# Optimization experiments

Measured on AMD Instinct MI355X. Metric: run time of the kernel, lower is better.

## Reference

```python
import jax, jax.numpy as jnp
import numpy as np

ROTARY_DIM = 32
THETA = 10000.0

def _rotate_half(t):
    # interleaved pairs: (..., d) -> rotate each (x1, x2) pair to (-x2, x1)
    x = t.reshape(t.shape[:-1] + (-1, 2))
    x1, x2 = x[..., 0], x[..., 1]
    return jnp.stack([-x2, x1], axis=-1).reshape(t.shape)

def _apply_rope(t, offset=0):
    # t: (B, h, T, dh); rotate only the first ROTARY_DIM dims
    T = t.shape[-2]
    inv_freq = 1.0 / (THETA ** (jnp.arange(0, ROTARY_DIM, 2, dtype=jnp.float32) / ROTARY_DIM))
    pos = jnp.arange(T, dtype=jnp.float32) + offset
    freqs = pos[:, None] * inv_freq[None, :]                 # (T, ROTARY_DIM/2)
    freqs = jnp.repeat(freqs, 2, axis=-1)                    # (T, ROTARY_DIM) interleaved
    cos, sin = jnp.cos(freqs), jnp.sin(freqs)
    t_rot, t_pass = t[..., :ROTARY_DIM], t[..., ROTARY_DIM:]
    t_rot = t_rot * cos + _rotate_half(t_rot) * sin
    return jnp.concatenate([t_rot, t_pass], axis=-1)

def setup_inputs() -> dict:
    key = jax.random.key(0)
    k1, k2, k3 = jax.random.split(key, 3)
    B, T, dim = 4, 1024, 1024
    x = jax.random.normal(k1, (B, T, dim), dtype=jnp.float32)
    Wqkv = jax.random.normal(k2, (dim, 3 * dim), dtype=jnp.float32) * (dim ** -0.5)
    Wout = jax.random.normal(k3, (dim, dim), dtype=jnp.float32) * (dim ** -0.5)
    return {"x": x, "Wqkv": Wqkv, "Wout": Wout}

def reference(x, Wqkv, Wout):
    B, T, dim = x.shape
    n_heads = 16
    dh = dim // n_heads
    qkv = x @ Wqkv                                            # (B, T, 3*dim)
    qkv = qkv.reshape(B, T, 3, n_heads, dh)
    qkv = jnp.transpose(qkv, (2, 0, 3, 1, 4))                 # (3, B, h, T, dh)
    q, k, v = qkv[0], qkv[1], qkv[2]
    q = _apply_rope(q, offset=0)
    k = _apply_rope(k, offset=0)
    scale = 1.0 / jnp.sqrt(jnp.asarray(dh, dtype=x.dtype))
    scores = jnp.einsum('bhqd,bhkd->bhqk', q, k) * scale      # (B, h, T, T)
    causal = jnp.tril(jnp.ones((T, T), dtype=bool))
    scores = jnp.where(causal, scores, jnp.asarray(-jnp.inf, dtype=scores.dtype))
    attn = jax.nn.softmax(scores, axis=-1)
    out = jnp.einsum('bhqk,bhkd->bhqd', attn, v)              # (B, h, T, dh)
    out = jnp.transpose(out, (0, 2, 1, 3)).reshape(B, T, dim)
    return out @ Wout
```

## Files before the change

kernel.cpp:

```cpp
#include <hip/hip_runtime.h>
#include <cstdint>
#include <cstddef>

typedef __bf16 bf16;
typedef __bf16 bf16x4 __attribute__((ext_vector_type(4)));
typedef __bf16 bf16x8 __attribute__((ext_vector_type(8)));
typedef float f32x4 __attribute__((ext_vector_type(4)));

#define DEVINL __device__ __forceinline__

static constexpr int Tn   = 1024;
static constexpr int DIM  = 1024;
static constexpr int NH   = 16;
static constexpr int DH   = 64;
static constexpr int QKVN = 3072;

DEVINL void g2l16(const void* g, void* l) {
  __builtin_amdgcn_global_load_lds(
      (const __attribute__((address_space(1))) void*)g,
      (__attribute__((address_space(3))) void*)l, 16, 0, 0);
}

__global__ void k_prep(const float* __restrict__ x, bf16* __restrict__ xb,
                       float2* __restrict__ tab,
                       const float* __restrict__ w1, bf16* __restrict__ o1,
                       const float* __restrict__ w2, bf16* __restrict__ o2) {
  __shared__ float tile[32][33];
  int bx = blockIdx.x;
  if (bx < 4096) {
    int i = bx * 256 + threadIdx.x;
    float4 v = reinterpret_cast<const float4*>(x)[i];
    bf16 o[4] = {(bf16)v.x, (bf16)v.y, (bf16)v.z, (bf16)v.w};
    reinterpret_cast<uint2*>(xb)[i] = *reinterpret_cast<uint2*>(o);
    return;
  }
  if (bx < 4160) {
    int e = (bx - 4096) * 256 + threadIdx.x;
    int t = e >> 4, fi = e & 15;
    float inv = exp2f(-(float)fi * 0.830482023721841f);
    float sn, cs;
    sincosf((float)t * inv, &sn, &cs);
    tab[e] = make_float2(cs, sn);
    return;
  }
  int sub = bx - 4160;
  const float* in; bf16* out; int N, n0, k0;
  if (sub < 3072) { in = w1; out = o1; N = 3072; n0 = (sub % 96) * 32; k0 = (sub / 96) * 32; }
  else { sub -= 3072; in = w2; out = o2; N = 1024; n0 = (sub & 31) * 32; k0 = (sub >> 5) * 32; }
  int tx = threadIdx.x & 31, ty = threadIdx.x >> 5;
#pragma unroll
  for (int j = 0; j < 32; j += 8)
    tile[ty + j][tx] = in[(size_t)(k0 + ty + j) * N + n0 + tx];
  __syncthreads();
#pragma unroll
  for (int j = 0; j < 32; j += 8)
    out[(size_t)(n0 + ty + j) * 1024 + k0 + tx] = (bf16)tile[tx][ty + j];
}

template <bool F32OUT, int BN, bool ROPE>
__global__ __launch_bounds__(256) void k_gemm_bt(
    const bf16* __restrict__ A, const bf16* __restrict__ Bt,
    void* __restrict__ Cp, bf16* __restrict__ vt, const float2* __restrict__ tab,
    int M, int N, int K) {
  constexpr int NI = BN / 32;
  constexpr int NB = BN / 32;
  __shared__ bf16 As[128 * 64];
  __shared__ bf16 Bs[BN * 64];
  const int tid  = threadIdx.x;
  const int wave = tid >> 6, lane = tid & 63;
  const int lrow = lane & 15, quad = lane >> 4;
  const int m0 = blockIdx.y * 128, n0 = blockIdx.x * BN;
  const int wm = (wave >> 1) * 64, wn = (wave & 1) * (BN / 2);

  const bf16* aP[4];
  const bf16* bP[NB];
#pragma unroll
  for (int i = 0; i < 4; i++) {
    int li = i * 256 + tid;
    int row = li >> 3, c = li & 7, gc = c ^ (row & 7);
    aP[i] = A + (size_t)(m0 + row) * K + gc * 8;
  }
#pragma unroll
  for (int i = 0; i < NB; i++) {
    int li = i * 256 + tid;
    int row = li >> 3, c = li & 7, gc = c ^ (row & 7);
    bP[i] = Bt + (size_t)(n0 + row) * K + gc * 8;
  }

  f32x4 acc[4][NI];
#pragma unroll
  for (int mi = 0; mi < 4; mi++)
#pragma unroll
    for (int ni = 0; ni < NI; ni++) acc[mi][ni] = 0.f;

  for (int k0 = 0; k0 < K; k0 += 64) {
    __syncthreads();
#pragma unroll
    for (int i = 0; i < 4; i++) {
      g2l16(aP[i], As + (i * 256 + tid) * 8);
      aP[i] += 64;
    }
#pragma unroll
    for (int i = 0; i < NB; i++) {
      g2l16(bP[i], Bs + (i * 256 + tid) * 8);
      bP[i] += 64;
    }
    __syncthreads();
#pragma unroll
    for (int ki = 0; ki < 2; ki++) {
      bf16x8 af[4], bfr[NI];
#pragma unroll
      for (int mi = 0; mi < 4; mi++) {
        int r = wm + mi * 16 + lrow;
        int pc = (ki * 4 + quad) ^ (r & 7);
        af[mi] = *reinterpret_cast<const bf16x8*>(As + r * 64 + pc * 8);
      }
#pragma unroll
      for (int ni = 0; ni < NI; ni++) {
        int r = wn + ni * 16 + lrow;
        int pc = (ki * 4 + quad) ^ (r & 7);
        bfr[ni] = *reinterpret_cast<const bf16x8*>(Bs + r * 64 + pc * 8);
      }
#pragma unroll
      for (int mi = 0; mi < 4; mi++)
#pragma unroll
        for (int ni = 0; ni < NI; ni++)
          acc[mi][ni] = __builtin_amdgcn_mfma_f32_16x16x32_bf16(bfr[ni], af[mi], acc[mi][ni], 0, 0, 0);
    }
  }

#pragma unroll
  for (int mi = 0; mi < 4; mi++) {
    const int row = m0 + wm + mi * 16 + lrow;
#pragma unroll
    for (int ni = 0; ni < NI; ni++) {
      const int colb = n0 + wn + ni * 16 + quad * 4;
      f32x4 v = acc[mi][ni];
      if (ROPE && colb >= 2 * DIM) {
        int t = row & (Tn - 1), bb = row >> 10;
        int hdb = colb - 2 * DIM;
#pragma unroll
        for (int r = 0; r < 4; r++)
          vt[((size_t)((bb << 10) + hdb + r) << 10) + t] = (bf16)v[r];
        continue;
      }
      if (ROPE && ((colb & 63) < 32)) {
        int t = row & (Tn - 1);
        int fi0 = (colb >> 1) & 15;
        float2 c0 = tab[(t << 4) + fi0];
        float2 c1 = tab[(t << 4) + fi0 + 1];
        float a0 = v[0], a1 = v[1], a2 = v[2], a3 = v[3];
        v[0] = a0 * c0.x - a1 * c0.y;
        v[1] = a1 * c0.x + a0 * c0.y;
        v[2] = a2 * c1.x - a3 * c1.y;
        v[3] = a3 * c1.x + a2 * c1.y;
      }
      if (F32OUT) {
        float4 st = {v[0], v[1], v[2], v[3]};
        *reinterpret_cast<float4*>(reinterpret_cast<float*>(Cp) + (size_t)row * N + colb) = st;
      } else {
        bf16x4 pk;
#pragma unroll
        for (int r = 0; r < 4; r++) pk[r] = (bf16)v[r];
        *reinterpret_cast<bf16x4*>(reinterpret_cast<bf16*>(Cp) + (size_t)row * N + colb) = pk;
      }
    }
  }
}

__global__ __launch_bounds__(256) void k_attn(
    const bf16* __restrict__ qkv, const bf16* __restrict__ vt,
    bf16* __restrict__ ao) {
  __shared__ bf16 Ks[2][64 * 64];
  __shared__ bf16 Vs[2][64 * 64];
  __shared__ bf16 Ps[4][16 * 64];

  const int tid  = threadIdx.x;
  const int wave = tid >> 6, lane = tid & 63;
  const int lrow = lane & 15, quad = lane >> 4;
  const int bh = blockIdx.y, b = bh >> 4, h = bh & 15;
  const int jn = blockIdx.x;
  const int jf = 15 - jn;
  const int qwf = jf * 64 + wave * 16;
  const int qwn = jn * 64 + wave * 16;
  const size_t qbase = (size_t)b * Tn * QKVN;

  bf16x8 qff[2], qfn[2];
  {
    const float SC = 0.125f * 1.44269504088896f;
    const bf16* qpf = qkv + qbase + (size_t)(qwf + lrow) * QKVN + h * DH;
    const bf16* qpn = qkv + qbase + (size_t)(qwn + lrow) * QKVN + h * DH;
    qff[0] = *reinterpret_cast<const bf16x8*>(qpf + quad * 8);
    qff[1] = *reinterpret_cast<const bf16x8*>(qpf + 32 + quad * 8);
    qfn[0] = *reinterpret_cast<const bf16x8*>(qpn + quad * 8);
    qfn[1] = *reinterpret_cast<const bf16x8*>(qpn + 32 + quad * 8);
#pragma unroll
    for (int j = 0; j < 8; j++) {
      qff[0][j] = (bf16)((float)qff[0][j] * SC);
      qff[1][j] = (bf16)((float)qff[1][j] * SC);
      qfn[0][j] = (bf16)((float)qfn[0][j] * SC);
      qfn[1][j] = (bf16)((float)qfn[1][j] * SC);
    }
  }

  f32x4 oaf[4], oan[4];
#pragma unroll
  for (int g = 0; g < 4; g++) { oaf[g] = 0.f; oan[g] = 0.f; }
  float lif = 0.f, lin = 0.f;

  const int ntiles = jf + 1;

  auto stage = [&](int k0, int bufi) {
#pragma unroll
    for (int i = 0; i < 2; i++) {
      int li2 = i * 256 + tid;
      int row = li2 >> 3, c = li2 & 7;
      int gc = c ^ (row & 7);
      g2l16(qkv + qbase + (size_t)(k0 + row) * QKVN + DIM + h * DH + gc * 8,
            &Ks[bufi][li2 * 8]);
      g2l16(vt + ((size_t)bh * DH + row) * Tn + k0 + gc * 8,
            &Vs[bufi][li2 * 8]);
    }
  };

  auto unit = [&](const bf16* ks, const bf16* vs, bf16x8 (&qf)[2], f32x4 (&oa)[4],
                  float& li, bool diag) {
    f32x4 s[4];
#pragma unroll
    for (int g = 0; g < 4; g++) s[g] = 0.f;
#pragma unroll
    for (int kh = 0; kh < 2; kh++) {
      const int cX = ((kh * 4 + quad) ^ (lrow & 7)) << 3;
#pragma unroll
      for (int g = 0; g < 4; g++) {
        bf16x8 kf = *reinterpret_cast<const bf16x8*>(ks + (g * 16 + lrow) * 64 + cX);
        s[g] = __builtin_amdgcn_mfma_f32_16x16x32_bf16(kf, qf[kh], s[g], 0, 0, 0);
      }
    }
    float psum = 0.f;
    const int qrel = wave * 16 + lrow;
#pragma unroll
    for (int g = 0; g < 4; g++) {
      bf16x4 pk;
#pragma unroll
      for (int r = 0; r < 4; r++) {
        float p = exp2f(s[g][r]);
        if (diag) {
          int kl = g * 16 + quad * 4 + r;
          p = (kl <= qrel) ? p : 0.f;
        }
        psum += p;
        pk[r] = (bf16)p;
      }
      int chunk = 2 * g + (quad >> 1);
      *reinterpret_cast<bf16x4*>(
          Ps[wave] + lrow * 64 + ((chunk ^ (lrow & 7)) << 3) + 4 * (quad & 1)) = pk;
    }
    li += psum;
#pragma unroll
    for (int kh = 0; kh < 2; kh++) {
      const int cX = ((kh * 4 + quad) ^ (lrow & 7)) << 3;
      bf16x8 pf = *reinterpret_cast<const bf16x8*>(Ps[wave] + lrow * 64 + cX);
#pragma unroll
      for (int g = 0; g < 4; g++) {
        bf16x8 vf = *reinterpret_cast<const bf16x8*>(vs + (g * 16 + lrow) * 64 + cX);
        oa[g] = __builtin_amdgcn_mfma_f32_16x16x32_bf16(pf, vf, oa[g], 0, 0, 0);
      }
    }
  };

  stage(0, 0);

  for (int kt = 0; kt < ntiles; kt++) {
    const int buf = kt & 1;
    __syncthreads();
    if (kt + 1 < ntiles) stage((kt + 1) << 6, buf ^ 1);

    const bf16* ks = Ks[buf];
    const bf16* vs = Vs[buf];

    unit(ks, vs, qff, oaf, lif, kt == jf);
    if (kt <= jn)
      unit(ks, vs, qfn, oan, lin, kt == jn);
  }

  lif += __shfl_xor(lif, 16, 64); lif += __shfl_xor(lif, 32, 64);
  lin += __shfl_xor(lin, 16, 64); lin += __shfl_xor(lin, 32, 64);

#pragma unroll
  for (int r = 0; r < 4; r++) {
    int m = quad * 4 + r;
    float invf = 1.0f / __shfl(lif, m, 64);
    float invn = 1.0f / __shfl(lin, m, 64);
    bf16* dstf = ao + ((size_t)b * Tn + qwf + m) * DIM + h * DH;
    bf16* dstn = ao + ((size_t)b * Tn + qwn + m) * DIM + h * DH;
    dstf[ 0 + lrow] = (bf16)(oaf[0][r] * invf);
    dstf[16 + lrow] = (bf16)(oaf[1][r] * invf);
    dstf[32 + lrow] = (bf16)(oaf[2][r] * invf);
    dstf[48 + lrow] = (bf16)(oaf[3][r] * invf);
    dstn[ 0 + lrow] = (bf16)(oan[0][r] * invn);
    dstn[16 + lrow] = (bf16)(oan[1][r] * invn);
    dstn[32 + lrow] = (bf16)(oan[2][r] * invn);
    dstn[48 + lrow] = (bf16)(oan[3][r] * invn);
  }
}

extern "C" void kernel_launch(void* const* d_in, const int* in_sizes, int n_in,
                              void* d_out, int out_size, void* d_ws, size_t ws_size,
                              hipStream_t stream) {
  const float* x    = (const float*)d_in[0];
  const float* Wqkv = (const float*)d_in[1];
  const float* Wout = (const float*)d_in[2];
  char* ws = (char*)d_ws;

  bf16*   xb    = (bf16*)(ws + 0);
  bf16*   wqkvT = (bf16*)(ws + 8388608);
  bf16*   woutT = (bf16*)(ws + 14680064);
  bf16*   qkv   = (bf16*)(ws + 16777216);
  bf16*   vt    = (bf16*)(ws + 41943040);
  bf16*   ao    = (bf16*)(ws + 50331648);
  float2* tab   = (float2*)(ws + 58720256);

  k_prep<<<8256, 256, 0, stream>>>(x, xb, tab, Wqkv, wqkvT, Wout, woutT);
  k_gemm_bt<false, 96, true><<<dim3(32, 32), 256, 0, stream>>>(
      xb, wqkvT, (void*)qkv, vt, tab, 4096, 3072, 1024);
  k_attn<<<dim3(8, 64), 256, 0, stream>>>(qkv, vt, ao);
  k_gemm_bt<true, 64, false><<<dim3(16, 32), 256, 0, stream>>>(
      ao, woutT, d_out, nullptr, nullptr, 4096, 1024, 1024);
  (void)in_sizes; (void)n_in; (void)out_size; (void)ws_size;
}
```

Measured before the change: 169.2 us.

## Split attention blocks into far/near wave pairs with 32-row query tiles

The attention kernel now handles two 32-row query tiles per block (one far, one near, each served by two waves) instead of two 64-row tiles processed by every wave. The grid doubles to 16x64 blocks, and each wave does only one unit per K/V tile, skipping compute once its own causal range is done. This gives more blocks and shorter per-block work, at the cost of loading K/V tiles twice as often per query row and leaving near waves idle during later iterations. Separately, the QKV GEMM tile width changes from 96 to 128 with a matching grid change.

```diff
diff --git a/kernel.cpp b/kernel.cpp
--- a/kernel.cpp
+++ b/kernel.cpp
@@ -180,35 +180,34 @@
   const int lrow = lane & 15, quad = lane >> 4;
   const int bh = blockIdx.y, b = bh >> 4, h = bh & 15;
   const int jn = blockIdx.x;
-  const int jf = 15 - jn;
-  const int qwf = jf * 64 + wave * 16;
-  const int qwn = jn * 64 + wave * 16;
+  const int jf = 31 - jn;
+  const bool isFar = wave < 2;
+  const int jmine = isFar ? jf : jn;
+  const int swave = wave & 1;
+  const int qw = jmine * 32 + swave * 16;
   const size_t qbase = (size_t)b * Tn * QKVN;
 
-  bf16x8 qff[2], qfn[2];
+  const int ntf = (jf >> 1) + 1;
+  const int myNt = (isFar ? ntf : ((jn >> 1) + 1));
+  const int qrel = (jmine & 1) * 32 + swave * 16 + lrow;
+
+  bf16x8 qf[2];
   {
     const float SC = 0.125f * 1.44269504088896f;
-    const bf16* qpf = qkv + qbase + (size_t)(qwf + lrow) * QKVN + h * DH;
-    const bf16* qpn = qkv + qbase + (size_t)(qwn + lrow) * QKVN + h * DH;
-    qff[0] = *reinterpret_cast<const bf16x8*>(qpf + quad * 8);
-    qff[1] = *reinterpret_cast<const bf16x8*>(qpf + 32 + quad * 8);
-    qfn[0] = *reinterpret_cast<const bf16x8*>(qpn + quad * 8);
-    qfn[1] = *reinterpret_cast<const bf16x8*>(qpn + 32 + quad * 8);
+    const bf16* qp = qkv + qbase + (size_t)(qw + lrow) * QKVN + h * DH;
+    qf[0] = *reinterpret_cast<const bf16x8*>(qp + quad * 8);
+    qf[1] = *reinterpret_cast<const bf16x8*>(qp + 32 + quad * 8);
 #pragma unroll
     for (int j = 0; j < 8; j++) {
-      qff[0][j] = (bf16)((float)qff[0][j] * SC);
-      qff[1][j] = (bf16)((float)qff[1][j] * SC);
-      qfn[0][j] = (bf16)((float)qfn[0][j] * SC);
-      qfn[1][j] = (bf16)((float)qfn[1][j] * SC);
-    }
-  }
-
-  f32x4 oaf[4], oan[4];
-#pragma unroll
-  for (int g = 0; g < 4; g++) { oaf[g] = 0.f; oan[g] = 0.f; }
-  float lif = 0.f, lin = 0.f;
-
-  const int ntiles = jf + 1;
+      qf[0][j] = (bf16)((float)qf[0][j] * SC);
+      qf[1][j] = (bf16)((float)qf[1][j] * SC);
+    }
+  }
+
+  f32x4 oa[4];
+#pragma unroll
+  for (int g = 0; g < 4; g++) oa[g] = 0.f;
+  float li = 0.f;
 
   auto stage = [&](int k0, int bufi) {
 #pragma unroll
@@ -223,85 +222,77 @@
     }
   };
 
-  auto unit = [&](const bf16* ks, const bf16* vs, bf16x8 (&qf)[2], f32x4 (&oa)[4],
-                  float& li, bool diag) {
-    f32x4 s[4];
-#pragma unroll
-    for (int g = 0; g < 4; g++) s[g] = 0.f;
-#pragma unroll
-    for (int kh = 0; kh < 2; kh++) {
-      const int cX = ((kh * 4 + quad) ^ (lrow & 7)) << 3;
-#pragma unroll
-      for (int g = 0; g < 4; g++) {
-        bf16x8 kf = *reinterpret_cast<const bf16x8*>(ks + (g * 16 + lrow) * 64 + cX);
-        s[g] = __builtin_amdgcn_mfma_f32_16x16x32_bf16(kf, qf[kh], s[g], 0, 0, 0);
-      }
-    }
-    float psum = 0.f;
-    const int qrel = wave * 16 + lrow;
-#pragma unroll
-    for (int g = 0; g < 4; g++) {
-      bf16x4 pk;
-#pragma unroll
-      for (int r = 0; r < 4; r++) {
-        float p = exp2f(s[g][r]);
-        if (diag) {
-          int kl = g * 16 + quad * 4 + r;
-          p = (kl <= qrel) ? p : 0.f;
-        }
-        psum += p;
-        pk[r] = (bf16)p;
-      }
-      int chunk = 2 * g + (quad >> 1);
-      *reinterpret_cast<bf16x4*>(
-          Ps[wave] + lrow * 64 + ((chunk ^ (lrow & 7)) << 3) + 4 * (quad & 1)) = pk;
-    }
-    li += psum;
-#pragma unroll
-    for (int kh = 0; kh < 2; kh++) {
-      const int cX = ((kh * 4 + quad) ^ (lrow & 7)) << 3;
-      bf16x8 pf = *reinterpret_cast<const bf16x8*>(Ps[wave] + lrow * 64 + cX);
-#pragma unroll
-      for (int g = 0; g < 4; g++) {
-        bf16x8 vf = *reinterpret_cast<const bf16x8*>(vs + (g * 16 + lrow) * 64 + cX);
-        oa[g] = __builtin_amdgcn_mfma_f32_16x16x32_bf16(pf, vf, oa[g], 0, 0, 0);
-      }
-    }
-  };
-
   stage(0, 0);
 
-  for (int kt = 0; kt < ntiles; kt++) {
+  for (int kt = 0; kt < ntf; kt++) {
     const int buf = kt & 1;
     __syncthreads();
-    if (kt + 1 < ntiles) stage((kt + 1) << 6, buf ^ 1);
-
-    const bf16* ks = Ks[buf];
-    const bf16* vs = Vs[buf];
-
-    unit(ks, vs, qff, oaf, lif, kt == jf);
-    if (kt <= jn)
-      unit(ks, vs, qfn, oan, lin, kt == jn);
-  }
-
-  lif += __shfl_xor(lif, 16, 64); lif += __shfl_xor(lif, 32, 64);
-  lin += __shfl_xor(lin, 16, 64); lin += __shfl_xor(lin, 32, 64);
+    if (kt + 1 < ntf) stage((kt + 1) << 6, buf ^ 1);
+
+    if (kt < myNt) {
+      const bf16* ks = Ks[buf];
+      const bf16* vs = Vs[buf];
+      const bool diag = (kt == myNt - 1);
+
+      f32x4 s[4];
+#pragma unroll
+      for (int g = 0; g < 4; g++) s[g] = 0.f;
+#pragma unroll
+      for (int kh = 0; kh < 2; kh++) {
+        const int cX = ((kh * 4 + quad) ^ (lrow & 7)) << 3;
+#pragma unroll
+        for (int g = 0; g < 4; g++) {
+          bf16x8 kf = *reinterpret_cast<const bf16x8*>(ks + (g * 16 + lrow) * 64 + cX);
+          s[g] = __builtin_amdgcn_mfma_f32_16x16x32_bf16(kf, qf[kh], s[g], 0, 0, 0);
+        }
+      }
+
+      float psum = 0.f;
+#pragma unroll
+      for (int g = 0; g < 4; g++) {
+        bf16x4 pk;
+#pragma unroll
+        for (int r = 0; r < 4; r++) {
+          float p = exp2f(s[g][r]);
+          if (diag) {
+            int kl = g * 16 + quad * 4 + r;
+            p = (kl <= qrel) ? p : 0.f;
+          }
+          psum += p;
+          pk[r] = (bf16)p;
+        }
+        int chunk = 2 * g + (quad >> 1);
+        *reinterpret_cast<bf16x4*>(
+            Ps[wave] + lrow * 64 + ((chunk ^ (lrow & 7)) << 3) + 4 * (quad & 1)) = pk;
+      }
+      li += psum;
+
+#pragma unroll
+      for (int kh = 0; kh < 2; kh++) {
+        const int cX = ((kh * 4 + quad) ^ (lrow & 7)) << 3;
+        bf16x8 pf = *reinterpret_cast<const bf16x8*>(Ps[wave] + lrow * 64 + cX);
+#pragma unroll
+        for (int g = 0; g < 4; g++) {
+          bf16x8 vf = *reinterpret_cast<const bf16x8*>(vs + (g * 16 + lrow) * 64 + cX);
+          oa[g] = __builtin_amdgcn_mfma_f32_16x16x32_bf16(pf, vf, oa[g], 0, 0, 0);
+        }
+      }
+    }
+  }
+
+  li += __shfl_xor(li, 16, 64);
+  li += __shfl_xor(li, 32, 64);
 
 #pragma unroll
   for (int r = 0; r < 4; r++) {
     int m = quad * 4 + r;
-    float invf = 1.0f / __shfl(lif, m, 64);
-    float invn = 1.0f / __shfl(lin, m, 64);
-    bf16* dstf = ao + ((size_t)b * Tn + qwf + m) * DIM + h * DH;
-    bf16* dstn = ao + ((size_t)b * Tn + qwn + m) * DIM + h * DH;
-    dstf[ 0 + lrow] = (bf16)(oaf[0][r] * invf);
-    dstf[16 + lrow] = (bf16)(oaf[1][r] * invf);
-    dstf[32 + lrow] = (bf16)(oaf[2][r] * invf);
-    dstf[48 + lrow] = (bf16)(oaf[3][r] * invf);
-    dstn[ 0 + lrow] = (bf16)(oan[0][r] * invn);
-    dstn[16 + lrow] = (bf16)(oan[1][r] * invn);
-    dstn[32 + lrow] = (bf16)(oan[2][r] * invn);
-    dstn[48 + lrow] = (bf16)(oan[3][r] * invn);
+    float inv = 1.0f / __shfl(li, m, 64);
+    int row = qw + m;
+    bf16* dst = ao + ((size_t)b * Tn + row) * DIM + h * DH;
+    dst[ 0 + lrow] = (bf16)(oa[0][r] * inv);
+    dst[16 + lrow] = (bf16)(oa[1][r] * inv);
+    dst[32 + lrow] = (bf16)(oa[2][r] * inv);
+    dst[48 + lrow] = (bf16)(oa[3][r] * inv);
   }
 }
 
@@ -322,9 +313,9 @@
   float2* tab   = (float2*)(ws + 58720256);
 
   k_prep<<<8256, 256, 0, stream>>>(x, xb, tab, Wqkv, wqkvT, Wout, woutT);
-  k_gemm_bt<false, 96, true><<<dim3(32, 32), 256, 0, stream>>>(
+  k_gemm_bt<false, 128, true><<<dim3(24, 32), 256, 0, stream>>>(
       xb, wqkvT, (void*)qkv, vt, tab, 4096, 3072, 1024);
-  k_attn<<<dim3(8, 64), 256, 0, stream>>>(qkv, vt, ao);
+  k_attn<<<dim3(16, 64), 256, 0, stream>>>(qkv, vt, ao);
   k_gemm_bt<true, 64, false><<<dim3(16, 32), 256, 0, stream>>>(
       ao, woutT, d_out, nullptr, nullptr, 4096, 1024, 1024);
   (void)in_sizes; (void)n_in; (void)out_size; (void)ws_size;
```

New measurement: 161.5 us. -4.5%, faster.
